# Optimization experiments

Hardware: AMD Instinct MI355X
Metric: run time of the kernel (lower is better)

Reference implementation:

```python
import jax, jax.numpy as jnp
import numpy as np

D = 16      # core_size
R = 8       # rank
SIZE = D ** 3  # 4096, nr_cores = 3


def setup_inputs() -> dict:
    key = jax.random.key(0)
    k = jax.random.split(key, 5)
    core_std = np.sqrt(2.0 / D).astype(np.float32)  # kaiming_normal over (-1, d, d)
    x = jax.random.normal(k[0], (8, 1024, SIZE), dtype=jnp.float32)
    core0 = core_std * jax.random.normal(k[1], (D, D, D, D, R, 1), dtype=jnp.float32)
    core1 = core_std * jax.random.normal(k[2], (D, D, D, D, R, R), dtype=jnp.float32)
    core2 = core_std * jax.random.normal(k[3], (D, D, D, D, 1, R), dtype=jnp.float32)
    bias = np.sqrt(1.0 / SIZE).astype(np.float32) * jax.random.uniform(
        k[4], (SIZE,), dtype=jnp.float32, minval=-1.0, maxval=1.0)
    return {"x": x, "core0": core0, "core1": core1, "core2": core2, "bias": bias}


def to_matrix(core0, core1, core2):
    # Faithful translation of BTT.to_matrix for nr_cores=3.
    # G starts as core0: (d,d,d,d,r,1)
    # step idx=0 (core1): j=d, i=d^2
    c1 = core1.reshape(D, D * D, D, R, R)          # jixcb
    g = core0.reshape(D, D * D, D, R, 1)           # jiyba
    G = jnp.einsum('jixcb,jiyba->jiyxca', c1, g)   # (d, d^2, d, d, r, 1)
    # step idx=1 (core2): j=d^2, i=d
    c2 = core2.reshape(D * D, D, D, 1, R)          # jixcb
    g = G.reshape(D * D, D, D * D, R, 1)           # jiyba
    G = jnp.einsum('jixcb,jiyba->jiyxca', c2, g)   # (d^2, d, d^2, d, 1, 1)
    return G.reshape(SIZE, SIZE)


def reference(x, core0, core1, core2, bias):
    G = to_matrix(core0, core1, core2)
    out = x.reshape(-1, SIZE) @ G + bias
    return out.reshape(x.shape)
```

## Files before the change

### kernel.cpp

```cpp
#include <hip/hip_runtime.h>
#include <stdint.h>

typedef unsigned short u16;
typedef short bf16x8 __attribute__((ext_vector_type(8)));
typedef float f32x4 __attribute__((ext_vector_type(4)));
typedef u16 u16x4 __attribute__((ext_vector_type(4)));

__device__ __forceinline__ u16 f2bf(float f) {
    union { float f; unsigned int i; } v; v.f = f;
    unsigned int x = v.i;
    return (u16)((x + 0x7FFFu + ((x >> 16) & 1u)) >> 16);
}

__device__ __forceinline__ void async_load16(const u16* g, u16* lds) {
    __builtin_amdgcn_global_load_lds(
        (const __attribute__((address_space(1))) unsigned int*)g,
        (__attribute__((address_space(3))) unsigned int*)lds,
        16, 0, 0);
}

__global__ void transpose_f32(const float* __restrict__ in, float* __restrict__ out,
                              int Q) {
    __shared__ float t[64][65];
    const int r0 = blockIdx.y * 64;
    const int q0 = blockIdx.x * 64;
    const int tx = threadIdx.x & 63;
    const int ty = threadIdx.x >> 6;
    #pragma unroll
    for (int k = 0; k < 16; ++k) {
        const int row = k * 4 + ty;
        t[row][tx] = in[(size_t)(r0 + row) * Q + q0 + tx];
    }
    __syncthreads();
    #pragma unroll
    for (int k = 0; k < 16; ++k) {
        const int qrow = k * 4 + ty;
        out[(size_t)(q0 + qrow) * 4096 + r0 + tx] = t[tx][qrow];
    }
}

__global__ void build_gt_t(const float* __restrict__ c0t, const float* __restrict__ c1t,
                           const float* __restrict__ c2t, u16* __restrict__ Gt) {
    int id = blockIdx.x;
    id = (id & 7) * 128 + (id >> 3);
    const int x1 = id >> 6;
    const int y1 = (id >> 2) & 15;
    const int p  = id & 3;
    const int r0 = p * 1024 + threadIdx.x * 4;
    const int colb = (y1 * 16 + x1) * 16;

    f32x4 a0[8];
    #pragma unroll
    for (int b = 0; b < 8; ++b)
        a0[b] = *(const f32x4*)(c0t + (size_t)(y1 * 8 + b) * 4096 + r0);

    f32x4 t[8];
    #pragma unroll
    for (int c = 0; c < 8; ++c) {
        f32x4 s = {0.f, 0.f, 0.f, 0.f};
        #pragma unroll
        for (int b = 0; b < 8; ++b) {
            f32x4 w = *(const f32x4*)(c1t + (size_t)(x1 * 64 + c * 8 + b) * 4096 + r0);
            s += w * a0[b];
        }
        t[c] = s;
    }
    #pragma unroll
    for (int x2 = 0; x2 < 16; ++x2) {
        f32x4 s = {0.f, 0.f, 0.f, 0.f};
        #pragma unroll
        for (int c = 0; c < 8; ++c) {
            f32x4 w = *(const f32x4*)(c2t + (size_t)(x2 * 8 + c) * 4096 + r0);
            s += w * t[c];
        }
        u16x4 o;
        #pragma unroll
        for (int j = 0; j < 4; ++j) o[j] = f2bf(s[j]);
        *(u16x4*)(Gt + (size_t)(colb + x2) * 4096 + r0) = o;
    }
}

__global__ void build_gt(const float* __restrict__ c0, const float* __restrict__ c1,
                         const float* __restrict__ c2, u16* __restrict__ Gt) {
    const int y1  = blockIdx.x >> 4;
    const int x1  = blockIdx.x & 15;
    const int r   = blockIdx.y * 256 + threadIdx.x;

    float a0[8];
    {
        f32x4 v0 = *(const f32x4*)(c0 + ((size_t)r * 16 + y1) * 8);
        f32x4 v1 = *(const f32x4*)(c0 + ((size_t)r * 16 + y1) * 8 + 4);
        #pragma unroll
        for (int b = 0; b < 4; ++b) { a0[b] = v0[b]; a0[4 + b] = v1[b]; }
    }
    float t[8];
    const float* c1row = c1 + ((size_t)r * 16 + x1) * 64;
    #pragma unroll
    for (int c = 0; c < 8; ++c) {
        f32x4 v0 = *(const f32x4*)(c1row + c * 8);
        f32x4 v1 = *(const f32x4*)(c1row + c * 8 + 4);
        float s = 0.f;
        #pragma unroll
        for (int b = 0; b < 4; ++b) s += v0[b] * a0[b] + v1[b] * a0[4 + b];
        t[c] = s;
    }
    const float* c2row = c2 + (size_t)r * 128;
    #pragma unroll
    for (int x2 = 0; x2 < 16; ++x2) {
        f32x4 v0 = *(const f32x4*)(c2row + x2 * 8);
        f32x4 v1 = *(const f32x4*)(c2row + x2 * 8 + 4);
        float s = 0.f;
        #pragma unroll
        for (int c = 0; c < 4; ++c) s += v0[c] * t[c] + v1[c] * t[4 + c];
        Gt[((size_t)(blockIdx.x * 16 + x2)) * 4096 + r] = f2bf(s);
    }
}

__global__ void conv_x(const f32x4* __restrict__ x, u16* __restrict__ xb, int n4) {
    for (int i = blockIdx.x * 256 + threadIdx.x; i < n4; i += gridDim.x * 256) {
        f32x4 v = x[i];
        u16x4 o;
        #pragma unroll
        for (int j = 0; j < 4; ++j) o[j] = f2bf(v[j]);
        *(u16x4*)(xb + 4 * (size_t)i) = o;
    }
}

__global__ __launch_bounds__(512, 2)
void gemm_8ph(const u16* __restrict__ Xb, const u16* __restrict__ Gt,
              const float* __restrict__ bias, float* __restrict__ out) {
    constexpr int K = 4096, N = 4096, NT = 64;
    extern __shared__ u16 lds[];

    const int tid  = threadIdx.x;
    const int lane = tid & 63;
    const int w    = tid >> 6;
    const int wmi  = w >> 2;
    const int wni  = w & 3;
    const int lr   = lane & 15;
    const int lq   = lane >> 4;
    const int xr   = lr & 7;

    int id = blockIdx.y * 16 + blockIdx.x;
    id = (id & 7) * 64 + (id >> 3);
    const int m0 = (id & 31) * 256;
    const int n0 = (id >> 5) * 256;

    const int r0 = tid >> 3;
    const int s0 = (tid & 7) ^ (r0 & 7);
    const int r1 = 64 + r0;
    const int s1 = ((512 + tid) & 7) ^ (r1 & 7);
    const size_t aoff0 = (size_t)(m0 + r0) * K + s0 * 8;
    const size_t aoff1 = (size_t)(m0 + r1) * K + s1 * 8;
    const size_t boff0 = (size_t)(n0 + r0) * K + s0 * 8;
    const size_t boff1 = (size_t)(n0 + r1) * K + s1 * 8;
    const int ldsw0 = (tid & ~63) * 8;
    const int ldsw1 = 4096 + (tid & ~63) * 8;

    const int aoffL = (wmi * 16 + lr) * 64;
    const int boffL = 16384 + (wni * 16 + lr) * 64;
    const int slot0 = (lq ^ xr) * 8;
    const int slot1 = ((4 + lq) ^ xr) * 8;

    f32x4 acc[8][4] = {};
    bf16x8 a[4][2];
    bf16x8 bfr[2][2][2];

    auto stageA = [&](int bb, int h, int t) {
        const u16* s = Xb + (size_t)h * (128 * K) + (size_t)t * 64;
        u16* d = lds + bb * 32768 + h * 8192;
        async_load16(s + aoff0, d + ldsw0);
        async_load16(s + aoff1, d + ldsw1);
    };
    auto stageB = [&](int bb, int h, int t) {
        const u16* s = Gt + (size_t)h * (128 * K) + (size_t)t * 64;
        u16* d = lds + bb * 32768 + 16384 + h * 8192;
        async_load16(s + boff0, d + ldsw0);
        async_load16(s + boff1, d + ldsw1);
    };
    auto loadA = [&](int bb, int h) {
        const u16* p = lds + bb * 32768 + h * 8192 + aoffL;
        #pragma unroll
        for (int li = 0; li < 4; ++li) {
            a[li][0] = *(const bf16x8*)(p + li * 2048 + slot0);
            a[li][1] = *(const bf16x8*)(p + li * 2048 + slot1);
        }
    };
    auto loadB = [&](int bb, int h) {
        const u16* p = lds + bb * 32768 + h * 8192 + boffL;
        #pragma unroll
        for (int lj = 0; lj < 2; ++lj) {
            bfr[h][lj][0] = *(const bf16x8*)(p + lj * 4096 + slot0);
            bfr[h][lj][1] = *(const bf16x8*)(p + lj * 4096 + slot1);
        }
    };
    auto mfmaQ = [&](int mh, int nh) {
        #pragma unroll
        for (int li = 0; li < 4; ++li)
            #pragma unroll
            for (int lj = 0; lj < 2; ++lj) {
                f32x4 c = acc[mh * 4 + li][nh * 2 + lj];
                c = __builtin_amdgcn_mfma_f32_16x16x32_bf16(a[li][0], bfr[nh][lj][0], c, 0, 0, 0);
                c = __builtin_amdgcn_mfma_f32_16x16x32_bf16(a[li][1], bfr[nh][lj][1], c, 0, 0, 0);
                acc[mh * 4 + li][nh * 2 + lj] = c;
            }
    };
    auto mfmaQ_refillA = [&](int mh, int nh, const u16* pA) {
        #pragma unroll
        for (int li = 0; li < 4; ++li) {
            #pragma unroll
            for (int lj = 0; lj < 2; ++lj) {
                f32x4 c = acc[mh * 4 + li][nh * 2 + lj];
                c = __builtin_amdgcn_mfma_f32_16x16x32_bf16(a[li][0], bfr[nh][lj][0], c, 0, 0, 0);
                c = __builtin_amdgcn_mfma_f32_16x16x32_bf16(a[li][1], bfr[nh][lj][1], c, 0, 0, 0);
                acc[mh * 4 + li][nh * 2 + lj] = c;
            }
            a[li][0] = *(const bf16x8*)(pA + li * 2048 + slot0);
            a[li][1] = *(const bf16x8*)(pA + li * 2048 + slot1);
        }
    };

    stageA(0, 0, 0); stageB(0, 0, 0); stageA(0, 1, 0); stageB(0, 1, 0);
    stageA(1, 0, 1); stageB(1, 0, 1); stageA(1, 1, 1); stageB(1, 1, 1);
    asm volatile("s_waitcnt vmcnt(8)" ::: "memory");
    __builtin_amdgcn_s_barrier();
    loadB(0, 1); loadA(0, 0); loadB(0, 0);

    for (int T = 0; T < NT; ++T) {
        const int bc = T & 1, bn = bc ^ 1;
        const int t2 = (T + 2) & (NT - 1);

        asm volatile("s_waitcnt lgkmcnt(0)" ::: "memory");
        __builtin_amdgcn_s_barrier();
        __builtin_amdgcn_sched_barrier(0);
        __builtin_amdgcn_s_setprio(1);
        mfmaQ(0, 0);
        __builtin_amdgcn_s_setprio(0);

        stageA(bc, 0, t2); stageB(bc, 0, t2);
        __builtin_amdgcn_s_setprio(1);
        mfmaQ_refillA(0, 1, lds + bc * 32768 + 8192 + aoffL);
        __builtin_amdgcn_s_setprio(0);

        asm volatile("s_waitcnt lgkmcnt(0)" ::: "memory");
        __builtin_amdgcn_s_barrier();
        __builtin_amdgcn_sched_barrier(0);
        __builtin_amdgcn_s_setprio(1);
        mfmaQ(1, 1);
        __builtin_amdgcn_s_setprio(0);

        stageA(bc, 1, t2); stageB(bc, 1, t2);
        asm volatile("s_waitcnt vmcnt(8)" ::: "memory");
        __builtin_amdgcn_s_barrier();
        __builtin_amdgcn_sched_barrier(0);
        loadB(bn, 1);
        __builtin_amdgcn_s_setprio(1);
        mfmaQ_refillA(1, 0, lds + bn * 32768 + aoffL);
        __builtin_amdgcn_s_setprio(0);
        loadB(bn, 0);
    }
    asm volatile("s_waitcnt vmcnt(0) lgkmcnt(0)" ::: "memory");

    #pragma unroll
    for (int j = 0; j < 4; ++j) {
        const int n = n0 + (j * 4 + wni) * 16 + lr;
        const float bv = bias[n];
        #pragma unroll
        for (int i = 0; i < 8; ++i) {
            const int mb = m0 + (2 * i + wmi) * 16 + lq * 4;
            #pragma unroll
            for (int r = 0; r < 4; ++r)
                out[(size_t)(mb + r) * N + n] = acc[i][j][r] + bv;
        }
    }
}

#define TM 128
#define TN 128
#define BK 32

__global__ void gemm_bt_f32(const float* __restrict__ Xf, const u16* __restrict__ Gt,
                            const float* __restrict__ bias, float* __restrict__ out) {
    constexpr int K = 4096, N = 4096;
    __shared__ __attribute__((aligned(16))) u16 As[TM * BK];
    __shared__ __attribute__((aligned(16))) u16 Bs[TN * BK];

    const int tid  = threadIdx.x;
    const int lane = tid & 63;
    const int w    = tid >> 6;
    const int m0   = blockIdx.y * TM;
    const int n0   = blockIdx.x * TN;
    const int wm   = (w >> 1) * 64;
    const int wn   = (w & 1) * 64;
    const int lr   = lane & 15;
    const int lk   = (lane >> 4) * 8;

    f32x4 acc[4][4] = {};

    const int srow   = tid >> 2;
    const int schunk = (tid & 3) * 8;
    const u16* grow0 = Gt + (size_t)(n0 + srow) * K + schunk;
    const u16* grow1 = Gt + (size_t)(n0 + 64 + srow) * K + schunk;
    u16* ldsB0 = &Bs[(tid & ~63) * 8];
    u16* ldsB1 = &Bs[(256 + (tid & ~63)) * 8];

    const float* xsrc = Xf + (size_t)(m0 + (tid >> 1)) * K + (tid & 1) * 16;
    u16* adst = &As[(tid >> 1) * BK + (tid & 1) * 16];

    for (int k0 = 0; k0 < K; k0 += BK) {
        __syncthreads();
        {
            f32x4 v0 = ((const f32x4*)(xsrc + k0))[0];
            f32x4 v1 = ((const f32x4*)(xsrc + k0))[1];
            f32x4 v2 = ((const f32x4*)(xsrc + k0))[2];
            f32x4 v3 = ((const f32x4*)(xsrc + k0))[3];
            bf16x8 w0, w1;
            #pragma unroll
            for (int j = 0; j < 4; ++j) {
                w0[j]     = (short)f2bf(v0[j]);
                w0[4 + j] = (short)f2bf(v1[j]);
                w1[j]     = (short)f2bf(v2[j]);
                w1[4 + j] = (short)f2bf(v3[j]);
            }
            *(bf16x8*)adst = w0;
            *(bf16x8*)(adst + 8) = w1;
        }
        async_load16(grow0 + k0, ldsB0);
        async_load16(grow1 + k0, ldsB1);
        __syncthreads();

        bf16x8 af[4], bg[4];
        #pragma unroll
        for (int i = 0; i < 4; ++i) {
            af[i] = *(const bf16x8*)(&As[(wm + i * 16 + lr) * BK + lk]);
            bg[i] = *(const bf16x8*)(&Bs[(wn + i * 16 + lr) * BK + lk]);
        }
        #pragma unroll
        for (int mt = 0; mt < 4; ++mt)
            #pragma unroll
            for (int nt = 0; nt < 4; ++nt)
                acc[mt][nt] = __builtin_amdgcn_mfma_f32_16x16x32_bf16(
                    af[mt], bg[nt], acc[mt][nt], 0, 0, 0);
    }

    #pragma unroll
    for (int nt = 0; nt < 4; ++nt) {
        const int n = n0 + wn + nt * 16 + lr;
        const float bv = bias[n];
        #pragma unroll
        for (int mt = 0; mt < 4; ++mt) {
            const int mbase = m0 + wm + mt * 16 + (lane >> 4) * 4;
            #pragma unroll
            for (int r = 0; r < 4; ++r) {
                out[(size_t)(mbase + r) * N + n] = acc[mt][nt][r] + bv;
            }
        }
    }
}

extern "C" void kernel_launch(void* const* d_in, const int* in_sizes, int n_in,
                              void* d_out, int out_size, void* d_ws, size_t ws_size,
                              hipStream_t stream) {
    const float* x    = (const float*)d_in[0];
    const float* c0   = (const float*)d_in[1];
    const float* c1   = (const float*)d_in[2];
    const float* c2   = (const float*)d_in[3];
    const float* bias = (const float*)d_in[4];
    float* out = (float*)d_out;

    const size_t GT_BYTES = (size_t)4096 * 4096 * sizeof(u16);
    const size_t XB_BYTES = (size_t)8192 * 4096 * sizeof(u16);
    u16* Gt = (u16*)d_ws;

    if (ws_size >= GT_BYTES + XB_BYTES) {
        char* scratch = (char*)d_ws + GT_BYTES;
        float* c1t = (float*)scratch;
        float* c0t = (float*)(scratch + (size_t)16 * 1024 * 1024);
        float* c2t = (float*)(scratch + (size_t)18 * 1024 * 1024);

        transpose_f32<<<dim3(16, 64), 256, 0, stream>>>(c1, c1t, 1024);
        transpose_f32<<<dim3(2, 64), 256, 0, stream>>>(c0, c0t, 128);
        transpose_f32<<<dim3(2, 64), 256, 0, stream>>>(c2, c2t, 128);
        build_gt_t<<<1024, 256, 0, stream>>>(c0t, c1t, c2t, Gt);

        u16* Xb = (u16*)((char*)d_ws + GT_BYTES);
        conv_x<<<8192, 256, 0, stream>>>((const f32x4*)x, Xb, 8192 * 4096 / 4);

        static int attr_done = 0;
        if (!attr_done) {
            hipFuncSetAttribute(reinterpret_cast<const void*>(gemm_8ph),
                                hipFuncAttributeMaxDynamicSharedMemorySize, 131072);
            attr_done = 1;
        }
        gemm_8ph<<<dim3(16, 32), 512, 131072, stream>>>(Xb, Gt, bias, out);
    } else {
        build_gt<<<dim3(256, 16), 256, 0, stream>>>(c0, c1, c2, Gt);
        gemm_bt_f32<<<dim3(32, 64), 256, 0, stream>>>(x, Gt, bias, out);
    }
}
```

Before: 498.7 us.

## Switch GEMM to 32x32x16 MFMA and fuse prep kernels into fewer launches

The main GEMM moves from 16x16x32 to 32x32x16 bf16 MFMA tiles, which changes the fragment layout, the LDS read pattern and the output store mapping. The block-index swizzle that grouped tiles is dropped in favour of a plain grid mapping. The three core transposes are merged into one launch, and the Gt build is fused with the x-to-bf16 conversion in a single kernel when the workspace has room, cutting launch overhead and letting the two overlap. The risks are more register pressure from the 16-wide accumulators and worse L2 locality without the swizzle.

```diff
diff --git a/kernel.cpp b/kernel.cpp
--- a/kernel.cpp
+++ b/kernel.cpp
@@ -4,6 +4,7 @@
 typedef unsigned short u16;
 typedef short bf16x8 __attribute__((ext_vector_type(8)));
 typedef float f32x4 __attribute__((ext_vector_type(4)));
+typedef float f32x16 __attribute__((ext_vector_type(16)));
 typedef u16 u16x4 __attribute__((ext_vector_type(4)));
 
 __device__ __forceinline__ u16 f2bf(float f) {
@@ -19,34 +20,36 @@
         16, 0, 0);
 }
 
-__global__ void transpose_f32(const float* __restrict__ in, float* __restrict__ out,
-                              int Q) {
+__global__ void transpose_cores(const float* __restrict__ c0, const float* __restrict__ c1,
+                                const float* __restrict__ c2, float* __restrict__ c0t,
+                                float* __restrict__ c1t, float* __restrict__ c2t) {
     __shared__ float t[64][65];
-    const int r0 = blockIdx.y * 64;
-    const int q0 = blockIdx.x * 64;
-    const int tx = threadIdx.x & 63;
-    const int ty = threadIdx.x >> 6;
-    #pragma unroll
-    for (int k = 0; k < 16; ++k) {
-        const int row = k * 4 + ty;
-        t[row][tx] = in[(size_t)(r0 + row) * Q + q0 + tx];
-    }
+    int b = blockIdx.x;
+    const float* in; float* outp; int Q, qt, rt;
+    if (b < 1024)      { in = c1; outp = c1t; Q = 1024; qt = b & 15;          rt = b >> 4; }
+    else if (b < 1152) { b -= 1024; in = c0; outp = c0t; Q = 128; qt = b & 1; rt = b >> 1; }
+    else               { b -= 1152; in = c2; outp = c2t; Q = 128; qt = b & 1; rt = b >> 1; }
+    const int r0 = rt * 64, q0 = qt * 64;
+    const int tx = threadIdx.x & 63, ty = threadIdx.x >> 6;
+    #pragma unroll
+    for (int k = 0; k < 16; ++k)
+        t[k * 4 + ty][tx] = in[(size_t)(r0 + k * 4 + ty) * Q + q0 + tx];
     __syncthreads();
     #pragma unroll
-    for (int k = 0; k < 16; ++k) {
-        const int qrow = k * 4 + ty;
-        out[(size_t)(q0 + qrow) * 4096 + r0 + tx] = t[tx][qrow];
-    }
-}
-
-__global__ void build_gt_t(const float* __restrict__ c0t, const float* __restrict__ c1t,
-                           const float* __restrict__ c2t, u16* __restrict__ Gt) {
-    int id = blockIdx.x;
-    id = (id & 7) * 128 + (id >> 3);
+    for (int k = 0; k < 16; ++k)
+        outp[(size_t)(q0 + k * 4 + ty) * 4096 + r0 + tx] = t[tx][k * 4 + ty];
+}
+
+__device__ __forceinline__ void build_body(int id_raw, int tid,
+                                           const float* __restrict__ c0t,
+                                           const float* __restrict__ c1t,
+                                           const float* __restrict__ c2t,
+                                           u16* __restrict__ Gt) {
+    int id = (id_raw & 7) * 128 + (id_raw >> 3);
     const int x1 = id >> 6;
     const int y1 = (id >> 2) & 15;
     const int p  = id & 3;
-    const int r0 = p * 1024 + threadIdx.x * 4;
+    const int r0 = p * 1024 + tid * 4;
     const int colb = (y1 * 16 + x1) * 16;
 
     f32x4 a0[8];
@@ -80,40 +83,9 @@
     }
 }
 
-__global__ void build_gt(const float* __restrict__ c0, const float* __restrict__ c1,
-                         const float* __restrict__ c2, u16* __restrict__ Gt) {
-    const int y1  = blockIdx.x >> 4;
-    const int x1  = blockIdx.x & 15;
-    const int r   = blockIdx.y * 256 + threadIdx.x;
-
-    float a0[8];
-    {
-        f32x4 v0 = *(const f32x4*)(c0 + ((size_t)r * 16 + y1) * 8);
-        f32x4 v1 = *(const f32x4*)(c0 + ((size_t)r * 16 + y1) * 8 + 4);
-        #pragma unroll
-        for (int b = 0; b < 4; ++b) { a0[b] = v0[b]; a0[4 + b] = v1[b]; }
-    }
-    float t[8];
-    const float* c1row = c1 + ((size_t)r * 16 + x1) * 64;
-    #pragma unroll
-    for (int c = 0; c < 8; ++c) {
-        f32x4 v0 = *(const f32x4*)(c1row + c * 8);
-        f32x4 v1 = *(const f32x4*)(c1row + c * 8 + 4);
-        float s = 0.f;
-        #pragma unroll
-        for (int b = 0; b < 4; ++b) s += v0[b] * a0[b] + v1[b] * a0[4 + b];
-        t[c] = s;
-    }
-    const float* c2row = c2 + (size_t)r * 128;
-    #pragma unroll
-    for (int x2 = 0; x2 < 16; ++x2) {
-        f32x4 v0 = *(const f32x4*)(c2row + x2 * 8);
-        f32x4 v1 = *(const f32x4*)(c2row + x2 * 8 + 4);
-        float s = 0.f;
-        #pragma unroll
-        for (int c = 0; c < 4; ++c) s += v0[c] * t[c] + v1[c] * t[4 + c];
-        Gt[((size_t)(blockIdx.x * 16 + x2)) * 4096 + r] = f2bf(s);
-    }
+__global__ void build_gt_t(const float* __restrict__ c0t, const float* __restrict__ c1t,
+                           const float* __restrict__ c2t, u16* __restrict__ Gt) {
+    build_body(blockIdx.x, threadIdx.x, c0t, c1t, c2t, Gt);
 }
 
 __global__ void conv_x(const f32x4* __restrict__ x, u16* __restrict__ xb, int n4) {
@@ -126,9 +98,26 @@
     }
 }
 
+__global__ void build_conv(const float* __restrict__ c0t, const float* __restrict__ c1t,
+                           const float* __restrict__ c2t, u16* __restrict__ Gt,
+                           const f32x4* __restrict__ x, u16* __restrict__ xb) {
+    if (blockIdx.x < 1024) {
+        build_body(blockIdx.x, threadIdx.x, c0t, c1t, c2t, Gt);
+    } else {
+        const int n4 = 8192 * 4096 / 4;
+        for (int i = (blockIdx.x - 1024) * 256 + threadIdx.x; i < n4; i += 3072 * 256) {
+            f32x4 v = x[i];
+            u16x4 o;
+            #pragma unroll
+            for (int j = 0; j < 4; ++j) o[j] = f2bf(v[j]);
+            *(u16x4*)(xb + 4 * (size_t)i) = o;
+        }
+    }
+}
+
 __global__ __launch_bounds__(512, 2)
-void gemm_8ph(const u16* __restrict__ Xb, const u16* __restrict__ Gt,
-              const float* __restrict__ bias, float* __restrict__ out) {
+void gemm_32(const u16* __restrict__ Xb, const u16* __restrict__ Gt,
+             const float* __restrict__ bias, float* __restrict__ out) {
     constexpr int K = 4096, N = 4096, NT = 64;
     extern __shared__ u16 lds[];
 
@@ -137,14 +126,12 @@
     const int w    = tid >> 6;
     const int wmi  = w >> 2;
     const int wni  = w & 3;
-    const int lr   = lane & 15;
-    const int lq   = lane >> 4;
-    const int xr   = lr & 7;
-
-    int id = blockIdx.y * 16 + blockIdx.x;
-    id = (id & 7) * 64 + (id >> 3);
-    const int m0 = (id & 31) * 256;
-    const int n0 = (id >> 5) * 256;
+    const int l31  = lane & 31;
+    const int l5   = lane >> 5;
+    const int l7   = lane & 7;
+
+    const int m0 = blockIdx.y * 256;
+    const int n0 = blockIdx.x * 256;
 
     const int r0 = tid >> 3;
     const int s0 = (tid & 7) ^ (r0 & 7);
@@ -157,14 +144,16 @@
     const int ldsw0 = (tid & ~63) * 8;
     const int ldsw1 = 4096 + (tid & ~63) * 8;
 
-    const int aoffL = (wmi * 16 + lr) * 64;
-    const int boffL = 16384 + (wni * 16 + lr) * 64;
-    const int slot0 = (lq ^ xr) * 8;
-    const int slot1 = ((4 + lq) ^ xr) * 8;
-
-    f32x4 acc[8][4] = {};
-    bf16x8 a[4][2];
-    bf16x8 bfr[2][2][2];
+    const int rowA0 = (0 + wmi) * 32 + l31;
+    const int rowA1 = (2 + wmi) * 32 + l31;
+    const int rowB  = wni * 32 + l31;
+    int slot[4];
+    #pragma unroll
+    for (int kk = 0; kk < 4; ++kk) slot[kk] = ((l5 + 2 * kk) ^ l7) * 8;
+
+    f32x16 acc[4][2] = {};
+    bf16x8 a[2][4];
+    bf16x8 bfr[2][4];
 
     auto stageA = [&](int bb, int h, int t) {
         const u16* s = Xb + (size_t)h * (128 * K) + (size_t)t * 64;
@@ -179,44 +168,36 @@
         async_load16(s + boff1, d + ldsw1);
     };
     auto loadA = [&](int bb, int h) {
-        const u16* p = lds + bb * 32768 + h * 8192 + aoffL;
-        #pragma unroll
-        for (int li = 0; li < 4; ++li) {
-            a[li][0] = *(const bf16x8*)(p + li * 2048 + slot0);
-            a[li][1] = *(const bf16x8*)(p + li * 2048 + slot1);
+        const u16* p = lds + bb * 32768 + h * 8192;
+        #pragma unroll
+        for (int kk = 0; kk < 4; ++kk) {
+            a[0][kk] = *(const bf16x8*)(p + rowA0 * 64 + slot[kk]);
+            a[1][kk] = *(const bf16x8*)(p + rowA1 * 64 + slot[kk]);
         }
     };
     auto loadB = [&](int bb, int h) {
-        const u16* p = lds + bb * 32768 + h * 8192 + boffL;
-        #pragma unroll
-        for (int lj = 0; lj < 2; ++lj) {
-            bfr[h][lj][0] = *(const bf16x8*)(p + lj * 4096 + slot0);
-            bfr[h][lj][1] = *(const bf16x8*)(p + lj * 4096 + slot1);
-        }
+        const u16* p = lds + bb * 32768 + 16384 + h * 8192;
+        #pragma unroll
+        for (int kk = 0; kk < 4; ++kk)
+            bfr[h][kk] = *(const bf16x8*)(p + rowB * 64 + slot[kk]);
     };
     auto mfmaQ = [&](int mh, int nh) {
         #pragma unroll
-        for (int li = 0; li < 4; ++li)
-            #pragma unroll
-            for (int lj = 0; lj < 2; ++lj) {
-                f32x4 c = acc[mh * 4 + li][nh * 2 + lj];
-                c = __builtin_amdgcn_mfma_f32_16x16x32_bf16(a[li][0], bfr[nh][lj][0], c, 0, 0, 0);
-                c = __builtin_amdgcn_mfma_f32_16x16x32_bf16(a[li][1], bfr[nh][lj][1], c, 0, 0, 0);
-                acc[mh * 4 + li][nh * 2 + lj] = c;
-            }
+        for (int kk = 0; kk < 4; ++kk)
+            #pragma unroll
+            for (int j = 0; j < 2; ++j)
+                acc[2 * mh + j][nh] = __builtin_amdgcn_mfma_f32_32x32x16_bf16(
+                    a[j][kk], bfr[nh][kk], acc[2 * mh + j][nh], 0, 0, 0);
     };
     auto mfmaQ_refillA = [&](int mh, int nh, const u16* pA) {
         #pragma unroll
-        for (int li = 0; li < 4; ++li) {
-            #pragma unroll
-            for (int lj = 0; lj < 2; ++lj) {
-                f32x4 c = acc[mh * 4 + li][nh * 2 + lj];
-                c = __builtin_amdgcn_mfma_f32_16x16x32_bf16(a[li][0], bfr[nh][lj][0], c, 0, 0, 0);
-                c = __builtin_amdgcn_mfma_f32_16x16x32_bf16(a[li][1], bfr[nh][lj][1], c, 0, 0, 0);
-                acc[mh * 4 + li][nh * 2 + lj] = c;
-            }
-            a[li][0] = *(const bf16x8*)(pA + li * 2048 + slot0);
-            a[li][1] = *(const bf16x8*)(pA + li * 2048 + slot1);
+        for (int kk = 0; kk < 4; ++kk) {
+            acc[2 * mh + 0][nh] = __builtin_amdgcn_mfma_f32_32x32x16_bf16(
+                a[0][kk], bfr[nh][kk], acc[2 * mh + 0][nh], 0, 0, 0);
+            acc[2 * mh + 1][nh] = __builtin_amdgcn_mfma_f32_32x32x16_bf16(
+                a[1][kk], bfr[nh][kk], acc[2 * mh + 1][nh], 0, 0, 0);
+            a[0][kk] = *(const bf16x8*)(pA + rowA0 * 64 + slot[kk]);
+            a[1][kk] = *(const bf16x8*)(pA + rowA1 * 64 + slot[kk]);
         }
     };
 
@@ -239,7 +220,7 @@
 
         stageA(bc, 0, t2); stageB(bc, 0, t2);
         __builtin_amdgcn_s_setprio(1);
-        mfmaQ_refillA(0, 1, lds + bc * 32768 + 8192 + aoffL);
+        mfmaQ_refillA(0, 1, lds + bc * 32768 + 8192);
         __builtin_amdgcn_s_setprio(0);
 
         asm volatile("s_waitcnt lgkmcnt(0)" ::: "memory");
@@ -255,23 +236,61 @@
         __builtin_amdgcn_sched_barrier(0);
         loadB(bn, 1);
         __builtin_amdgcn_s_setprio(1);
-        mfmaQ_refillA(1, 0, lds + bn * 32768 + aoffL);
+        mfmaQ_refillA(1, 0, lds + bn * 32768);
         __builtin_amdgcn_s_setprio(0);
         loadB(bn, 0);
     }
     asm volatile("s_waitcnt vmcnt(0) lgkmcnt(0)" ::: "memory");
 
     #pragma unroll
-    for (int j = 0; j < 4; ++j) {
-        const int n = n0 + (j * 4 + wni) * 16 + lr;
+    for (int nj = 0; nj < 2; ++nj) {
+        const int n = n0 + (nj * 4 + wni) * 32 + l31;
         const float bv = bias[n];
         #pragma unroll
-        for (int i = 0; i < 8; ++i) {
-            const int mb = m0 + (2 * i + wmi) * 16 + lq * 4;
-            #pragma unroll
-            for (int r = 0; r < 4; ++r)
-                out[(size_t)(mb + r) * N + n] = acc[i][j][r] + bv;
-        }
+        for (int i = 0; i < 4; ++i) {
+            const int mbase = m0 + (i * 2 + wmi) * 32 + 4 * l5;
+            #pragma unroll
+            for (int r = 0; r < 16; ++r) {
+                const int row = mbase + (r & 3) + 8 * (r >> 2);
+                out[(size_t)row * N + n] = acc[i][nj][r] + bv;
+            }
+        }
+    }
+}
+
+__global__ void build_gt(const float* __restrict__ c0, const float* __restrict__ c1,
+                         const float* __restrict__ c2, u16* __restrict__ Gt) {
+    const int y1  = blockIdx.x >> 4;
+    const int x1  = blockIdx.x & 15;
+    const int r   = blockIdx.y * 256 + threadIdx.x;
+
+    float a0[8];
+    {
+        f32x4 v0 = *(const f32x4*)(c0 + ((size_t)r * 16 + y1) * 8);
+        f32x4 v1 = *(const f32x4*)(c0 + ((size_t)r * 16 + y1) * 8 + 4);
+        #pragma unroll
+        for (int b = 0; b < 4; ++b) { a0[b] = v0[b]; a0[4 + b] = v1[b]; }
+    }
+    float t[8];
+    const float* c1row = c1 + ((size_t)r * 16 + x1) * 64;
+    #pragma unroll
+    for (int c = 0; c < 8; ++c) {
+        f32x4 v0 = *(const f32x4*)(c1row + c * 8);
+        f32x4 v1 = *(const f32x4*)(c1row + c * 8 + 4);
+        float s = 0.f;
+        #pragma unroll
+        for (int b = 0; b < 4; ++b) s += v0[b] * a0[b] + v1[b] * a0[4 + b];
+        t[c] = s;
+    }
+    const float* c2row = c2 + (size_t)r * 128;
+    #pragma unroll
+    for (int x2 = 0; x2 < 16; ++x2) {
+        f32x4 v0 = *(const f32x4*)(c2row + x2 * 8);
+        f32x4 v1 = *(const f32x4*)(c2row + x2 * 8 + 4);
+        float s = 0.f;
+        #pragma unroll
+        for (int c = 0; c < 4; ++c) s += v0[c] * t[c] + v1[c] * t[4 + c];
+        Gt[((size_t)(blockIdx.x * 16 + x2)) * 4096 + r] = f2bf(s);
     }
 }
 
@@ -368,31 +387,38 @@
     const float* bias = (const float*)d_in[4];
     float* out = (float*)d_out;
 
-    const size_t GT_BYTES = (size_t)4096 * 4096 * sizeof(u16);
-    const size_t XB_BYTES = (size_t)8192 * 4096 * sizeof(u16);
+    const size_t GT_BYTES   = (size_t)4096 * 4096 * sizeof(u16);
+    const size_t XB_BYTES   = (size_t)8192 * 4096 * sizeof(u16);
+    const size_t CORE_BYTES = (size_t)20 * 1024 * 1024;
     u16* Gt = (u16*)d_ws;
 
     if (ws_size >= GT_BYTES + XB_BYTES) {
-        char* scratch = (char*)d_ws + GT_BYTES;
-        float* c1t = (float*)scratch;
-        float* c0t = (float*)(scratch + (size_t)16 * 1024 * 1024);
-        float* c2t = (float*)(scratch + (size_t)18 * 1024 * 1024);
-
-        transpose_f32<<<dim3(16, 64), 256, 0, stream>>>(c1, c1t, 1024);
-        transpose_f32<<<dim3(2, 64), 256, 0, stream>>>(c0, c0t, 128);
-        transpose_f32<<<dim3(2, 64), 256, 0, stream>>>(c2, c2t, 128);
-        build_gt_t<<<1024, 256, 0, stream>>>(c0t, c1t, c2t, Gt);
-
         u16* Xb = (u16*)((char*)d_ws + GT_BYTES);
-        conv_x<<<8192, 256, 0, stream>>>((const f32x4*)x, Xb, 8192 * 4096 / 4);
-
         static int attr_done = 0;
         if (!attr_done) {
-            hipFuncSetAttribute(reinterpret_cast<const void*>(gemm_8ph),
+            hipFuncSetAttribute(reinterpret_cast<const void*>(gemm_32),
                                 hipFuncAttributeMaxDynamicSharedMemorySize, 131072);
             attr_done = 1;
         }
-        gemm_8ph<<<dim3(16, 32), 512, 131072, stream>>>(Xb, Gt, bias, out);
+
+        if (ws_size >= GT_BYTES + XB_BYTES + CORE_BYTES) {
+            char* cores = (char*)d_ws + GT_BYTES + XB_BYTES;
+            float* c1t = (float*)cores;
+            float* c0t = (float*)(cores + (size_t)16 * 1024 * 1024);
+            float* c2t = (float*)(cores + (size_t)18 * 1024 * 1024);
+            transpose_cores<<<1280, 256, 0, stream>>>(c0, c1, c2, c0t, c1t, c2t);
+            build_conv<<<4096, 256, 0, stream>>>(c0t, c1t, c2t, Gt,
+                                                 (const f32x4*)x, Xb);
+        } else {
+            char* scratch = (char*)d_ws + GT_BYTES;
+            float* c1t = (float*)scratch;
+            float* c0t = (float*)(scratch + (size_t)16 * 1024 * 1024);
+            float* c2t = (float*)(scratch + (size_t)18 * 1024 * 1024);
+            transpose_cores<<<1280, 256, 0, stream>>>(c0, c1, c2, c0t, c1t, c2t);
+            build_gt_t<<<1024, 256, 0, stream>>>(c0t, c1t, c2t, Gt);
+            conv_x<<<8192, 256, 0, stream>>>((const f32x4*)x, Xb, 8192 * 4096 / 4);
+        }
+        gemm_32<<<dim3(16, 32), 512, 131072, stream>>>(Xb, Gt, bias, out);
     } else {
         build_gt<<<dim3(256, 16), 256, 0, stream>>>(c0, c1, c2, Gt);
         gemm_bt_f32<<<dim3(32, 64), 256, 0, stream>>>(x, Gt, bias, out);
```

Measured after the change: 523.3 us. 4.9% more time.

## Reuse core1 in registers across y1 when building G and fuse core transposes

Applied to the files above, without the earlier changes.

Replaces the per-(y1,x1) G-construction kernel with one where each thread loads its 64 core1 values once and reuses them across all 16 y1 slices, cutting redundant core1 reads. The three core transposes are merged into a single launch to cut launch overhead. Transposed cores move to a separate workspace region when space allows. The new build kernel runs only 256 blocks with high register use, which risks poor latency hiding.

```diff
diff --git a/kernel.cpp b/kernel.cpp
--- a/kernel.cpp
+++ b/kernel.cpp
@@ -19,100 +19,70 @@
         16, 0, 0);
 }
 
-__global__ void transpose_f32(const float* __restrict__ in, float* __restrict__ out,
-                              int Q) {
+__global__ void transpose_cores(const float* __restrict__ c0, const float* __restrict__ c1,
+                                const float* __restrict__ c2, float* __restrict__ c0t,
+                                float* __restrict__ c1t, float* __restrict__ c2t) {
     __shared__ float t[64][65];
-    const int r0 = blockIdx.y * 64;
-    const int q0 = blockIdx.x * 64;
-    const int tx = threadIdx.x & 63;
-    const int ty = threadIdx.x >> 6;
-    #pragma unroll
-    for (int k = 0; k < 16; ++k) {
-        const int row = k * 4 + ty;
-        t[row][tx] = in[(size_t)(r0 + row) * Q + q0 + tx];
-    }
+    int b = blockIdx.x;
+    const float* in; float* outp; int Q, qt, rt;
+    if (b < 1024)      { in = c1; outp = c1t; Q = 1024; qt = b & 15;          rt = b >> 4; }
+    else if (b < 1152) { b -= 1024; in = c0; outp = c0t; Q = 128; qt = b & 1; rt = b >> 1; }
+    else               { b -= 1152; in = c2; outp = c2t; Q = 128; qt = b & 1; rt = b >> 1; }
+    const int r0 = rt * 64, q0 = qt * 64;
+    const int tx = threadIdx.x & 63, ty = threadIdx.x >> 6;
+    #pragma unroll
+    for (int k = 0; k < 16; ++k)
+        t[k * 4 + ty][tx] = in[(size_t)(r0 + k * 4 + ty) * Q + q0 + tx];
     __syncthreads();
     #pragma unroll
-    for (int k = 0; k < 16; ++k) {
-        const int qrow = k * 4 + ty;
-        out[(size_t)(q0 + qrow) * 4096 + r0 + tx] = t[tx][qrow];
-    }
-}
-
-__global__ void build_gt_t(const float* __restrict__ c0t, const float* __restrict__ c1t,
-                           const float* __restrict__ c2t, u16* __restrict__ Gt) {
-    int id = blockIdx.x;
-    id = (id & 7) * 128 + (id >> 3);
-    const int x1 = id >> 6;
-    const int y1 = (id >> 2) & 15;
-    const int p  = id & 3;
-    const int r0 = p * 1024 + threadIdx.x * 4;
-    const int colb = (y1 * 16 + x1) * 16;
-
-    f32x4 a0[8];
-    #pragma unroll
-    for (int b = 0; b < 8; ++b)
-        a0[b] = *(const f32x4*)(c0t + (size_t)(y1 * 8 + b) * 4096 + r0);
-
-    f32x4 t[8];
-    #pragma unroll
-    for (int c = 0; c < 8; ++c) {
-        f32x4 s = {0.f, 0.f, 0.f, 0.f};
-        #pragma unroll
-        for (int b = 0; b < 8; ++b) {
-            f32x4 w = *(const f32x4*)(c1t + (size_t)(x1 * 64 + c * 8 + b) * 4096 + r0);
-            s += w * a0[b];
-        }
-        t[c] = s;
-    }
-    #pragma unroll
-    for (int x2 = 0; x2 < 16; ++x2) {
-        f32x4 s = {0.f, 0.f, 0.f, 0.f};
-        #pragma unroll
-        for (int c = 0; c < 8; ++c) {
-            f32x4 w = *(const f32x4*)(c2t + (size_t)(x2 * 8 + c) * 4096 + r0);
-            s += w * t[c];
-        }
-        u16x4 o;
-        #pragma unroll
-        for (int j = 0; j < 4; ++j) o[j] = f2bf(s[j]);
-        *(u16x4*)(Gt + (size_t)(colb + x2) * 4096 + r0) = o;
-    }
-}
-
-__global__ void build_gt(const float* __restrict__ c0, const float* __restrict__ c1,
-                         const float* __restrict__ c2, u16* __restrict__ Gt) {
-    const int y1  = blockIdx.x >> 4;
-    const int x1  = blockIdx.x & 15;
-    const int r   = blockIdx.y * 256 + threadIdx.x;
-
-    float a0[8];
-    {
-        f32x4 v0 = *(const f32x4*)(c0 + ((size_t)r * 16 + y1) * 8);
-        f32x4 v1 = *(const f32x4*)(c0 + ((size_t)r * 16 + y1) * 8 + 4);
-        #pragma unroll
-        for (int b = 0; b < 4; ++b) { a0[b] = v0[b]; a0[4 + b] = v1[b]; }
-    }
-    float t[8];
-    const float* c1row = c1 + ((size_t)r * 16 + x1) * 64;
-    #pragma unroll
-    for (int c = 0; c < 8; ++c) {
-        f32x4 v0 = *(const f32x4*)(c1row + c * 8);
-        f32x4 v1 = *(const f32x4*)(c1row + c * 8 + 4);
-        float s = 0.f;
-        #pragma unroll
-        for (int b = 0; b < 4; ++b) s += v0[b] * a0[b] + v1[b] * a0[4 + b];
-        t[c] = s;
-    }
-    const float* c2row = c2 + (size_t)r * 128;
-    #pragma unroll
-    for (int x2 = 0; x2 < 16; ++x2) {
-        f32x4 v0 = *(const f32x4*)(c2row + x2 * 8);
-        f32x4 v1 = *(const f32x4*)(c2row + x2 * 8 + 4);
-        float s = 0.f;
-        #pragma unroll
-        for (int c = 0; c < 4; ++c) s += v0[c] * t[c] + v1[c] * t[4 + c];
-        Gt[((size_t)(blockIdx.x * 16 + x2)) * 4096 + r] = f2bf(s);
+    for (int k = 0; k < 16; ++k)
+        outp[(size_t)(q0 + k * 4 + ty) * 4096 + r0 + tx] = t[tx][k * 4 + ty];
+}
+
+__global__ __launch_bounds__(256, 1)
+void build_gt_reuse(const float* __restrict__ c0t, const float* __restrict__ c1t,
+                    const float* __restrict__ c2t, u16* __restrict__ Gt) {
+    const int x1 = blockIdx.x;
+    const int r  = blockIdx.y * 256 + threadIdx.x;
+
+    float c1v[64];
+    #pragma unroll
+    for (int q = 0; q < 64; ++q)
+        c1v[q] = c1t[(size_t)(x1 * 64 + q) * 4096 + r];
+
+    #pragma unroll
+    for (int yh = 0; yh < 2; ++yh) {
+        float t[8][8];
+        #pragma unroll
+        for (int yy = 0; yy < 8; ++yy) {
+            const int y1 = yh * 8 + yy;
+            float a0[8];
+            #pragma unroll
+            for (int b = 0; b < 8; ++b)
+                a0[b] = c0t[(size_t)(y1 * 8 + b) * 4096 + r];
+            #pragma unroll
+            for (int c = 0; c < 8; ++c) {
+                float s = 0.f;
+                #pragma unroll
+                for (int b = 0; b < 8; ++b) s += c1v[c * 8 + b] * a0[b];
+                t[yy][c] = s;
+            }
+        }
+        #pragma unroll
+        for (int x2 = 0; x2 < 16; ++x2) {
+            float c2v[8];
+            #pragma unroll
+            for (int c = 0; c < 8; ++c)
+                c2v[c] = c2t[(size_t)(x2 * 8 + c) * 4096 + r];
+            #pragma unroll
+            for (int yy = 0; yy < 8; ++yy) {
+                const int y1 = yh * 8 + yy;
+                float s = 0.f;
+                #pragma unroll
+                for (int c = 0; c < 8; ++c) s += c2v[c] * t[yy][c];
+                Gt[(size_t)((y1 * 16 + x1) * 16 + x2) * 4096 + r] = f2bf(s);
+            }
+        }
     }
 }
 
@@ -275,6 +245,42 @@
     }
 }
 
+__global__ void build_gt(const float* __restrict__ c0, const float* __restrict__ c1,
+                         const float* __restrict__ c2, u16* __restrict__ Gt) {
+    const int y1  = blockIdx.x >> 4;
+    const int x1  = blockIdx.x & 15;
+    const int r   = blockIdx.y * 256 + threadIdx.x;
+
+    float a0[8];
+    {
+        f32x4 v0 = *(const f32x4*)(c0 + ((size_t)r * 16 + y1) * 8);
+        f32x4 v1 = *(const f32x4*)(c0 + ((size_t)r * 16 + y1) * 8 + 4);
+        #pragma unroll
+        for (int b = 0; b < 4; ++b) { a0[b] = v0[b]; a0[4 + b] = v1[b]; }
+    }
+    float t[8];
+    const float* c1row = c1 + ((size_t)r * 16 + x1) * 64;
+    #pragma unroll
+    for (int c = 0; c < 8; ++c) {
+        f32x4 v0 = *(const f32x4*)(c1row + c * 8);
+        f32x4 v1 = *(const f32x4*)(c1row + c * 8 + 4);
+        float s = 0.f;
+        #pragma unroll
+        for (int b = 0; b < 4; ++b) s += v0[b] * a0[b] + v1[b] * a0[4 + b];
+        t[c] = s;
+    }
+    const float* c2row = c2 + (size_t)r * 128;
+    #pragma unroll
+    for (int x2 = 0; x2 < 16; ++x2) {
+        f32x4 v0 = *(const f32x4*)(c2row + x2 * 8);
+        f32x4 v1 = *(const f32x4*)(c2row + x2 * 8 + 4);
+        float s = 0.f;
+        #pragma unroll
+        for (int c = 0; c < 4; ++c) s += v0[c] * t[c] + v1[c] * t[4 + c];
+        Gt[((size_t)(blockIdx.x * 16 + x2)) * 4096 + r] = f2bf(s);
+    }
+}
+
 #define TM 128
 #define TN 128
 #define BK 32
@@ -368,30 +374,35 @@
     const float* bias = (const float*)d_in[4];
     float* out = (float*)d_out;
 
-    const size_t GT_BYTES = (size_t)4096 * 4096 * sizeof(u16);
-    const size_t XB_BYTES = (size_t)8192 * 4096 * sizeof(u16);
+    const size_t GT_BYTES   = (size_t)4096 * 4096 * sizeof(u16);
+    const size_t XB_BYTES   = (size_t)8192 * 4096 * sizeof(u16);
+    const size_t CORE_BYTES = (size_t)20 * 1024 * 1024;
     u16* Gt = (u16*)d_ws;
 
     if (ws_size >= GT_BYTES + XB_BYTES) {
-        char* scratch = (char*)d_ws + GT_BYTES;
-        float* c1t = (float*)scratch;
-        float* c0t = (float*)(scratch + (size_t)16 * 1024 * 1024);
-        float* c2t = (float*)(scratch + (size_t)18 * 1024 * 1024);
-
-        transpose_f32<<<dim3(16, 64), 256, 0, stream>>>(c1, c1t, 1024);
-        transpose_f32<<<dim3(2, 64), 256, 0, stream>>>(c0, c0t, 128);
-        transpose_f32<<<dim3(2, 64), 256, 0, stream>>>(c2, c2t, 128);
-        build_gt_t<<<1024, 256, 0, stream>>>(c0t, c1t, c2t, Gt);
-
         u16* Xb = (u16*)((char*)d_ws + GT_BYTES);
-        conv_x<<<8192, 256, 0, stream>>>((const f32x4*)x, Xb, 8192 * 4096 / 4);
-
         static int attr_done = 0;
         if (!attr_done) {
             hipFuncSetAttribute(reinterpret_cast<const void*>(gemm_8ph),
                                 hipFuncAttributeMaxDynamicSharedMemorySize, 131072);
             attr_done = 1;
         }
+
+        float* c1t; float* c0t; float* c2t;
+        if (ws_size >= GT_BYTES + XB_BYTES + CORE_BYTES) {
+            char* cores = (char*)d_ws + GT_BYTES + XB_BYTES;
+            c1t = (float*)cores;
+            c0t = (float*)(cores + (size_t)16 * 1024 * 1024);
+            c2t = (float*)(cores + (size_t)18 * 1024 * 1024);
+        } else {
+            char* scratch = (char*)d_ws + GT_BYTES;
+            c1t = (float*)scratch;
+            c0t = (float*)(scratch + (size_t)16 * 1024 * 1024);
+            c2t = (float*)(scratch + (size_t)18 * 1024 * 1024);
+        }
+        transpose_cores<<<1280, 256, 0, stream>>>(c0, c1, c2, c0t, c1t, c2t);
+        build_gt_reuse<<<dim3(16, 16), 256, 0, stream>>>(c0t, c1t, c2t, Gt);
+        conv_x<<<8192, 256, 0, stream>>>((const f32x4*)x, Xb, 8192 * 4096 / 4);
         gemm_8ph<<<dim3(16, 32), 512, 131072, stream>>>(Xb, Gt, bias, out);
     } else {
         build_gt<<<dim3(256, 16), 256, 0, stream>>>(c0, c1, c2, Gt);
```

Result: no change. 498.1 us (-0.1%).
